# Kernel tuning notes

Measured on AMD Instinct MI355X. Metric: run time of the kernel, lower is better.

The kernel has to match this reference:

```python
import jax, jax.numpy as jnp
import numpy as np

EPS_ATTN = 1e-6
LN_EPS = 1e-5

def _layernorm(x, g, b):
    mu = jnp.mean(x, axis=-1, keepdims=True)
    var = jnp.var(x, axis=-1, keepdims=True)
    return (x - mu) * jax.lax.rsqrt(var + LN_EPS) * g + b

def _phi(x):
    return jax.nn.elu(x) + 1.0

def setup_inputs() -> dict:
    key = jax.random.key(0)
    ks = jax.random.split(key, 8)
    B, T, D, H = 2, 4096, 128, 128  # D = token_dim = d+1, H = hidden_dim
    s = 0.02
    return {
        "tokens": jax.random.normal(ks[0], (B, T, D), dtype=jnp.float32),
        "Wq": jax.random.normal(ks[1], (D, H), dtype=jnp.float32) * s,
        "Wk": jax.random.normal(ks[2], (D, H), dtype=jnp.float32) * s,
        "Wv": jax.random.normal(ks[3], (D, D), dtype=jnp.float32) * s,
        "Wg": jax.random.normal(ks[4], (D, D), dtype=jnp.float32) * s,
        "bg": jnp.zeros((D,), dtype=jnp.float32),
        "Wo": jax.random.normal(ks[5], (D, D), dtype=jnp.float32) * s,
        "g1": jnp.ones((D,), dtype=jnp.float32),
        "b1": jnp.zeros((D,), dtype=jnp.float32),
        "g2": jnp.ones((D,), dtype=jnp.float32),
        "b2": jnp.zeros((D,), dtype=jnp.float32),
    }

def reference(tokens, Wq, Wk, Wv, Wg, bg, Wo, g1, b1, g2, b2):
    x = _layernorm(tokens, g1, b1)                 # (b,t,m)
    Q = x @ Wq                                     # (b,t,h)
    K = x @ Wk                                     # (b,t,h)
    V = x @ Wv                                     # (b,t,m)
    G = jax.nn.sigmoid(x @ Wg + bg)                # (b,t,m)
    Vg = V * G
    Qp = _phi(Q)
    Kp = _phi(K)
    # causal linear attention via cumulative outer products
    kv = jnp.einsum('bth,btm->bthm', Kp, Vg)       # (b,t,h,m)
    S_kv = jnp.cumsum(kv, axis=1)
    S_k = jnp.cumsum(Kp, axis=1)
    numerator = jnp.einsum('bth,bthm->btm', Qp, S_kv)
    denom = jnp.maximum(jnp.einsum('bth,bth->bt', Qp, S_k), EPS_ATTN)
    attn_out = numerator / denom[..., None]
    out = tokens + (attn_out @ Wo) * 0.1
    return _layernorm(out, g2, b2)
```

## Files before the change

### kernel.cpp

```cpp
#include <hip/hip_runtime.h>
#include <math.h>

#define T_ 4096
#define D_ 128
#define NTOK 8192
#define CHUNK 64
#define NCB 64
#define NCH 128
#define LN_EPS 1e-5f
#define EPS_ATTN 1e-6f

typedef __attribute__((ext_vector_type(8))) short bf16x8;
typedef __attribute__((ext_vector_type(4))) short bf16x4;
typedef __attribute__((ext_vector_type(2))) short bf16x2;
typedef __attribute__((ext_vector_type(4))) float f32x4;

__device__ inline short f2bf(float f) {
  unsigned u = __builtin_bit_cast(unsigned, f);
  u += 0x7fffu + ((u >> 16) & 1u);
  return (short)(u >> 16);
}
__device__ inline float bf2f(short s) {
  unsigned u = ((unsigned)(unsigned short)s) << 16;
  return __builtin_bit_cast(float, u);
}
__device__ inline float phi_(float x) { return x > 0.f ? x + 1.f : __expf(x); }

__global__ __launch_bounds__(256) void k_prep(const float* __restrict__ in,
    const float* __restrict__ g, const float* __restrict__ b,
    short* __restrict__ xb) {
  const int w = threadIdx.x >> 6, l = threadIdx.x & 63;
  const int tok = blockIdx.x*4 + w;
  const float2 v = *(const float2*)&in[tok*D_ + l*2];
  float s = v.x + v.y, q = v.x*v.x + v.y*v.y;
  #pragma unroll
  for (int off = 32; off; off >>= 1) { s += __shfl_xor(s, off); q += __shfl_xor(q, off); }
  const float mean = s*(1.f/D_);
  const float r = rsqrtf(q*(1.f/D_) - mean*mean + LN_EPS);
  const float2 gg = *(const float2*)&g[l*2];
  const float2 bb = *(const float2*)&b[l*2];
  bf16x2 o;
  o.x = f2bf((v.x-mean)*r*gg.x + bb.x);
  o.y = f2bf((v.y-mean)*r*gg.y + bb.y);
  *(bf16x2*)&xb[tok*D_ + l*2] = o;
}

__global__ __launch_bounds__(256) void k_wprep(const float* __restrict__ Wq,
    const float* __restrict__ Wk, const float* __restrict__ Wv,
    const float* __restrict__ Wg, const float* __restrict__ Wo,
    short* __restrict__ WT) {
  const float* W = blockIdx.x==0?Wq: blockIdx.x==1?Wk: blockIdx.x==2?Wv: blockIdx.x==3?Wg:Wo;
  short* out = WT + blockIdx.x*D_*D_;
  __shared__ float lds[128][132];
  const int tid = threadIdx.x;
  #pragma unroll
  for (int it = 0; it < 16; ++it) {
    const int f = it*1024 + tid*4;
    const int k = f >> 7, n = f & 127;
    const float4 v = *(const float4*)&W[f];
    lds[k][n] = v.x; lds[k][n+1] = v.y; lds[k][n+2] = v.z; lds[k][n+3] = v.w;
  }
  __syncthreads();
  #pragma unroll
  for (int it = 0; it < 16; ++it) {
    const int f = it*1024 + tid*4;
    const int n = f >> 7, k = f & 127;
    bf16x4 o;
    o.x = f2bf(lds[k][n]);   o.y = f2bf(lds[k+1][n]);
    o.z = f2bf(lds[k+2][n]); o.w = f2bf(lds[k+3][n]);
    *(bf16x4*)&out[f] = o;
  }
}

__global__ __launch_bounds__(256) void k_qkvg(const short* __restrict__ xb,
    const short* __restrict__ WT,
    short* __restrict__ Qp, short* __restrict__ Kp, short* __restrict__ KpT,
    short* __restrict__ VT, short* __restrict__ GT) {
  const int m0 = blockIdx.x * 64;
  const int y = blockIdx.y;
  const int tid = threadIdx.x;
  __shared__ short xs[64][136];
  __shared__ short wsd[128][136];
  const short* W = WT + y*D_*D_;
  #pragma unroll
  for (int u = tid; u < 1024; u += 256) {
    const int r = u >> 4, c8 = (u & 15)*8;
    *(bf16x8*)&xs[r][c8] = *(const bf16x8*)&xb[(m0+r)*D_ + c8];
  }
  #pragma unroll
  for (int u = tid; u < 2048; u += 256) {
    const int r = u >> 4, c8 = (u & 15)*8;
    *(bf16x8*)&wsd[r][c8] = *(const bf16x8*)&W[r*D_ + c8];
  }
  __syncthreads();
  const int w = tid >> 6, l = tid & 63;
  const int i = l & 15, q = l >> 4;
  f32x4 acc[4][2];
  #pragma unroll
  for (int mt = 0; mt < 4; ++mt)
    #pragma unroll
    for (int nt = 0; nt < 2; ++nt) acc[mt][nt] = (f32x4){0.f,0.f,0.f,0.f};
  #pragma unroll
  for (int kk = 0; kk < 4; ++kk) {
    bf16x8 a[4], bfr[2];
    #pragma unroll
    for (int mt = 0; mt < 4; ++mt) a[mt] = *(const bf16x8*)&xs[mt*16+i][kk*32+q*8];
    #pragma unroll
    for (int nt = 0; nt < 2; ++nt) bfr[nt] = *(const bf16x8*)&wsd[w*32+nt*16+i][kk*32+q*8];
    #pragma unroll
    for (int mt = 0; mt < 4; ++mt)
      #pragma unroll
      for (int nt = 0; nt < 2; ++nt)
        acc[mt][nt] = __builtin_amdgcn_mfma_f32_16x16x32_bf16(a[mt], bfr[nt], acc[mt][nt], 0, 0, 0);
  }
  if (y == 0) {
    #pragma unroll
    for (int mt = 0; mt < 4; ++mt)
      #pragma unroll
      for (int nt = 0; nt < 2; ++nt) {
        const int h = w*32 + nt*16 + i;
        #pragma unroll
        for (int r = 0; r < 4; ++r) {
          const int t = m0 + mt*16 + 4*q + r;
          Qp[t*D_ + h] = f2bf(phi_(acc[mt][nt][r]));
        }
      }
  } else if (y == 1) {
    #pragma unroll
    for (int mt = 0; mt < 4; ++mt)
      #pragma unroll
      for (int nt = 0; nt < 2; ++nt) {
        const int h = w*32 + nt*16 + i;
        const int t0 = m0 + mt*16 + 4*q;
        bf16x4 o;
        #pragma unroll
        for (int r = 0; r < 4; ++r) {
          const float pv = phi_(acc[mt][nt][r]);
          const short bv = f2bf(pv);
          Kp[(t0+r)*D_ + h] = bv;
          o[r] = bv;
        }
        *(bf16x4*)&KpT[h*NTOK + t0] = o;
      }
  } else {
    short* dst = (y == 2) ? VT : GT;
    #pragma unroll
    for (int mt = 0; mt < 4; ++mt)
      #pragma unroll
      for (int nt = 0; nt < 2; ++nt) {
        const int h = w*32 + nt*16 + i;
        const int t0 = m0 + mt*16 + 4*q;
        bf16x4 o;
        #pragma unroll
        for (int r = 0; r < 4; ++r) o[r] = f2bf(acc[mt][nt][r]);
        *(bf16x4*)&dst[h*NTOK + t0] = o;
      }
  }
}

__global__ __launch_bounds__(256) void k_chunkkv(const short* __restrict__ KpT,
    const short* __restrict__ VT, const short* __restrict__ GT,
    const float* __restrict__ bg,
    float* __restrict__ KVT, float* __restrict__ Ksum) {
  const int c = blockIdx.x, hh = blockIdx.y;
  const int tid = threadIdx.x;
  const int tb = c*CHUNK;
  __shared__ short vgl[128][72];
  __shared__ short kpl[64][72];
  __shared__ float ksp[64][5];
  #pragma unroll
  for (int u = tid; u < 1024; u += 256) {
    const int d = u >> 3, c8 = (u & 7)*8;
    bf16x8 v  = *(const bf16x8*)&VT[d*NTOK + tb + c8];
    bf16x8 g8 = *(const bf16x8*)&GT[d*NTOK + tb + c8];
    const float bgd = bg[d];
    bf16x8 o;
    #pragma unroll
    for (int j = 0; j < 8; ++j) {
      const float gv = 1.f/(1.f + __expf(-(bf2f(g8[j]) + bgd)));
      o[j] = f2bf(bf2f(v[j]) * gv);
    }
    *(bf16x8*)&vgl[d][c8] = o;
  }
  #pragma unroll
  for (int u = tid; u < 512; u += 256) {
    const int h = u >> 3, c8 = (u & 7)*8;
    *(bf16x8*)&kpl[h][c8] = *(const bf16x8*)&KpT[(hh*64+h)*NTOK + tb + c8];
  }
  __syncthreads();
  const int w = tid >> 6, l = tid & 63, i = l & 15, q = l >> 4;
  f32x4 acc[2][4];
  #pragma unroll
  for (int mt = 0; mt < 2; ++mt)
    #pragma unroll
    for (int nt = 0; nt < 4; ++nt) acc[mt][nt] = (f32x4){0.f,0.f,0.f,0.f};
  #pragma unroll
  for (int kk = 0; kk < 2; ++kk) {
    bf16x8 a[2], bb[4];
    #pragma unroll
    for (int mt = 0; mt < 2; ++mt) a[mt] = *(const bf16x8*)&vgl[(2*w+mt)*16+i][kk*32+q*8];
    #pragma unroll
    for (int nt = 0; nt < 4; ++nt) bb[nt] = *(const bf16x8*)&kpl[nt*16+i][kk*32+q*8];
    #pragma unroll
    for (int mt = 0; mt < 2; ++mt)
      #pragma unroll
      for (int nt = 0; nt < 4; ++nt)
        acc[mt][nt] = __builtin_amdgcn_mfma_f32_16x16x32_bf16(a[mt], bb[nt], acc[mt][nt], 0, 0, 0);
  }
  float* KVc = KVT + (size_t)c*16384;
  #pragma unroll
  for (int mt = 0; mt < 2; ++mt)
    #pragma unroll
    for (int nt = 0; nt < 4; ++nt)
      #pragma unroll
      for (int r = 0; r < 4; ++r) {
        const int d = (2*w+mt)*16 + 4*q + r;
        const int h = hh*64 + nt*16 + i;
        KVc[d*128 + h] = acc[mt][nt][r];
      }
  {
    const int h = tid >> 2, part = tid & 3;
    float s = 0.f;
    #pragma unroll
    for (int t = 0; t < 16; ++t) s += bf2f(kpl[h][part*16 + t]);
    ksp[h][part] = s;
  }
  __syncthreads();
  if (tid < 64)
    Ksum[c*128 + hh*64 + tid] = ksp[tid][0]+ksp[tid][1]+ksp[tid][2]+ksp[tid][3];
}

__global__ __launch_bounds__(256) void k_prefix(const float* __restrict__ KVT,
    short* __restrict__ KVTb, float* __restrict__ Ksum) {
  const int tid = threadIdx.x;
  if (blockIdx.x < 128) {
    const int b = blockIdx.x >> 6;
    const int e = (blockIdx.x & 63)*256 + tid;
    const size_t base = (size_t)b*NCB*16384 + e;
    float run = 0.f;
    #pragma unroll 8
    for (int c = 0; c < NCB; ++c) {
      const float v = KVT[base + (size_t)c*16384];
      KVTb[base + (size_t)c*16384] = f2bf(run);
      run += v;
    }
  } else if (tid < 128) {
    const int b = blockIdx.x - 128;
    float run = 0.f;
    #pragma unroll 8
    for (int c = 0; c < NCB; ++c) {
      const int idx = (b*NCB + c)*128 + tid;
      const float v = Ksum[idx];
      Ksum[idx] = run;
      run += v;
    }
  }
}

__global__ __launch_bounds__(256) void k_scores(const short* __restrict__ Qp,
    const short* __restrict__ Kp, const float* __restrict__ Ksum,
    short* __restrict__ A, float* __restrict__ den) {
  const int c = blockIdx.x, tid = threadIdx.x;
  const int tb = c*CHUNK;
  __shared__ short qpl[64][136], kpl[64][136];
  __shared__ float ksl[128], rsl[64];
  #pragma unroll
  for (int u = tid; u < 1024; u += 256) {
    const int t = u >> 4, c8 = (u & 15)*8;
    *(bf16x8*)&qpl[t][c8] = *(const bf16x8*)&Qp[(tb+t)*D_ + c8];
    *(bf16x8*)&kpl[t][c8] = *(const bf16x8*)&Kp[(tb+t)*D_ + c8];
  }
  if (tid < 128) ksl[tid] = Ksum[c*128 + tid];
  __syncthreads();
  const int w = tid >> 6, l = tid & 63, i = l & 15, q = l >> 4;
  f32x4 acc[4];
  #pragma unroll
  for (int nt = 0; nt < 4; ++nt) acc[nt] = (f32x4){0.f,0.f,0.f,0.f};
  #pragma unroll
  for (int kk = 0; kk < 4; ++kk) {
    bf16x8 a = *(const bf16x8*)&qpl[w*16+i][kk*32+q*8];
    for (int nt = 0; nt <= w; ++nt) {
      bf16x8 bb = *(const bf16x8*)&kpl[nt*16+i][kk*32+q*8];
      acc[nt] = __builtin_amdgcn_mfma_f32_16x16x32_bf16(a, bb, acc[nt], 0, 0, 0);
    }
  }
  short* Ac = A + c*4096;
  float rs[4] = {0.f,0.f,0.f,0.f};
  #pragma unroll
  for (int nt = 0; nt < 4; ++nt) {
    #pragma unroll
    for (int r = 0; r < 4; ++r) {
      const int t = w*16 + 4*q + r;
      const int s = nt*16 + i;
      const float v = (nt <= w && s <= t) ? acc[nt][r] : 0.f;
      rs[r] += v;
      Ac[t*64 + s] = f2bf(v);
    }
  }
  #pragma unroll
  for (int r = 0; r < 4; ++r) {
    #pragma unroll
    for (int off = 1; off < 16; off <<= 1) rs[r] += __shfl_xor(rs[r], off);
  }
  if (i == 0) {
    #pragma unroll
    for (int r = 0; r < 4; ++r) rsl[w*16 + 4*q + r] = rs[r];
  }
  __syncthreads();
  if (tid < 64) {
    float dot = 0.f;
    #pragma unroll 8
    for (int h = 0; h < 128; ++h) dot += bf2f(qpl[tid][h]) * ksl[h];
    den[c*64 + tid] = rsl[tid] + dot;
  }
}

__global__ __launch_bounds__(256) void k_attnout(const short* __restrict__ Aintra,
    const short* __restrict__ Qp, const short* __restrict__ VT,
    const short* __restrict__ GT, const float* __restrict__ bg,
    const short* __restrict__ KVTb, const float* __restrict__ den,
    short* __restrict__ attn) {
  const int c = blockIdx.x, dh = blockIdx.y, tid = threadIdx.x;
  const int tb = c*CHUNK;
  __shared__ short at[64][200], bt[64][200];
  __shared__ float denl[64];
  const short* Ac = Aintra + c*4096;
  #pragma unroll
  for (int u = tid; u < 512; u += 256) {
    const int t = u >> 3, c8 = (u & 7)*8;
    *(bf16x8*)&at[t][c8] = *(const bf16x8*)&Ac[t*64 + c8];
  }
  #pragma unroll
  for (int u = tid; u < 1024; u += 256) {
    const int t = u >> 4, c8 = (u & 15)*8;
    *(bf16x8*)&at[t][64 + c8] = *(const bf16x8*)&Qp[(tb+t)*D_ + c8];
  }
  #pragma unroll
  for (int u = tid; u < 512; u += 256) {
    const int dd = u >> 3, c8 = (u & 7)*8;
    const int d = dh*64 + dd;
    bf16x8 v  = *(const bf16x8*)&VT[d*NTOK + tb + c8];
    bf16x8 g8 = *(const bf16x8*)&GT[d*NTOK + tb + c8];
    const float bgd = bg[d];
    bf16x8 o;
    #pragma unroll
    for (int j = 0; j < 8; ++j) {
      const float gv = 1.f/(1.f + __expf(-(bf2f(g8[j]) + bgd)));
      o[j] = f2bf(bf2f(v[j]) * gv);
    }
    *(bf16x8*)&bt[dd][c8] = o;
  }
  #pragma unroll
  for (int u = tid; u < 1024; u += 256) {
    const int dd = u >> 4, c8 = (u & 15)*8;
    *(bf16x8*)&bt[dd][64 + c8] = *(const bf16x8*)&KVTb[(size_t)c*16384 + (dh*64+dd)*128 + c8];
  }
  if (tid < 64) denl[tid] = den[c*64 + tid];
  __syncthreads();
  const int w = tid >> 6, l = tid & 63, i = l & 15, q = l >> 4;
  f32x4 acc[4];
  #pragma unroll
  for (int nt = 0; nt < 4; ++nt) acc[nt] = (f32x4){0.f,0.f,0.f,0.f};
  #pragma unroll
  for (int kk = 0; kk < 6; ++kk) {
    bf16x8 a = *(const bf16x8*)&at[w*16+i][kk*32+q*8];
    #pragma unroll
    for (int nt = 0; nt < 4; ++nt) {
      bf16x8 bb = *(const bf16x8*)&bt[nt*16+i][kk*32+q*8];
      acc[nt] = __builtin_amdgcn_mfma_f32_16x16x32_bf16(a, bb, acc[nt], 0, 0, 0);
    }
  }
  #pragma unroll
  for (int r = 0; r < 4; ++r) {
    const int t = w*16 + 4*q + r;
    const float inv = 1.f / fmaxf(denl[t], EPS_ATTN);
    #pragma unroll
    for (int nt = 0; nt < 4; ++nt)
      attn[(size_t)(tb+t)*D_ + dh*64 + nt*16 + i] = f2bf(acc[nt][r] * inv);
  }
}

__global__ __launch_bounds__(256) void k_outln2(const short* __restrict__ attn,
    const short* __restrict__ WoT, const float* __restrict__ tokens,
    const float* __restrict__ g2, const float* __restrict__ b2,
    float* __restrict__ out) {
  const int m0 = blockIdx.x*32, tid = threadIdx.x;
  __shared__ short al[32][136], wl[128][136];
  __shared__ float tl[32][132];
  __shared__ float suml[32][2], ssql[32][2];
  __shared__ float meanl[32], rstdl[32];
  __shared__ float gl[128], bl2[128];
  #pragma unroll
  for (int u = tid; u < 512; u += 256) {
    const int t = u >> 4, c8 = (u & 15)*8;
    *(bf16x8*)&al[t][c8] = *(const bf16x8*)&attn[(m0+t)*D_ + c8];
  }
  #pragma unroll
  for (int u = tid; u < 2048; u += 256) {
    const int n = u >> 4, c8 = (u & 15)*8;
    *(bf16x8*)&wl[n][c8] = *(const bf16x8*)&WoT[n*D_ + c8];
  }
  #pragma unroll
  for (int u = tid; u < 1024; u += 256) {
    const int t = u >> 5, c4 = (u & 31)*4;
    *(float4*)&tl[t][c4] = *(const float4*)&tokens[(m0+t)*D_ + c4];
  }
  if (tid < 128) { gl[tid] = g2[tid]; bl2[tid] = b2[tid]; }
  __syncthreads();
  const int w = tid >> 6, l = tid & 63, i = l & 15, q = l >> 4;
  const int mt = w >> 1, nh = w & 1;
  f32x4 acc[4];
  #pragma unroll
  for (int j = 0; j < 4; ++j) acc[j] = (f32x4){0.f,0.f,0.f,0.f};
  #pragma unroll
  for (int kk = 0; kk < 4; ++kk) {
    bf16x8 a = *(const bf16x8*)&al[mt*16+i][kk*32+q*8];
    #pragma unroll
    for (int j = 0; j < 4; ++j) {
      bf16x8 bb = *(const bf16x8*)&wl[(nh*4+j)*16+i][kk*32+q*8];
      acc[j] = __builtin_amdgcn_mfma_f32_16x16x32_bf16(a, bb, acc[j], 0, 0, 0);
    }
  }
  float p[4][4], ps[4], qs[4];
  #pragma unroll
  for (int r = 0; r < 4; ++r) {
    const int t = mt*16 + 4*q + r;
    ps[r] = 0.f; qs[r] = 0.f;
    #pragma unroll
    for (int j = 0; j < 4; ++j) {
      const int col = nh*64 + j*16 + i;
      const float v = tl[t][col] + 0.1f*acc[j][r];
      p[r][j] = v; ps[r] += v; qs[r] += v*v;
    }
  }
  #pragma unroll
  for (int r = 0; r < 4; ++r) {
    #pragma unroll
    for (int off = 1; off < 16; off <<= 1) {
      ps[r] += __shfl_xor(ps[r], off);
      qs[r] += __shfl_xor(qs[r], off);
    }
  }
  if (i == 0) {
    #pragma unroll
    for (int r = 0; r < 4; ++r) {
      suml[mt*16+4*q+r][nh] = ps[r];
      ssql[mt*16+4*q+r][nh] = qs[r];
    }
  }
  __syncthreads();
  if (tid < 32) {
    const float s = suml[tid][0] + suml[tid][1];
    const float qq = ssql[tid][0] + ssql[tid][1];
    const float mean = s*(1.f/D_);
    meanl[tid] = mean;
    rstdl[tid] = rsqrtf(qq*(1.f/D_) - mean*mean + LN_EPS);
  }
  __syncthreads();
  #pragma unroll
  for (int r = 0; r < 4; ++r) {
    const int t = mt*16 + 4*q + r;
    const float mean = meanl[t], rr = rstdl[t];
    #pragma unroll
    for (int j = 0; j < 4; ++j) {
      const int col = nh*64 + j*16 + i;
      out[(m0+t)*D_ + col] = (p[r][j]-mean)*rr*gl[col] + bl2[col];
    }
  }
}

extern "C" void kernel_launch(void* const* d_in, const int* in_sizes, int n_in,
                              void* d_out, int out_size, void* d_ws, size_t ws_size,
                              hipStream_t stream) {
  const float* tokens = (const float*)d_in[0];
  const float* Wq = (const float*)d_in[1];
  const float* Wk = (const float*)d_in[2];
  const float* Wv = (const float*)d_in[3];
  const float* Wg = (const float*)d_in[4];
  const float* bg = (const float*)d_in[5];
  const float* Wo = (const float*)d_in[6];
  const float* g1 = (const float*)d_in[7];
  const float* b1 = (const float*)d_in[8];
  const float* g2 = (const float*)d_in[9];
  const float* b2 = (const float*)d_in[10];

  char* base = (char*)d_ws;
  short* xb     = (short*)(base);
  short* Qp     = (short*)(base + (2u<<20));
  short* Kp     = (short*)(base + (4u<<20));
  short* KpT    = (short*)(base + (6u<<20));
  short* VT     = (short*)(base + (8u<<20));
  short* GT     = (short*)(base + (10u<<20));
  short* attn   = (short*)(base + (12u<<20));
  short* KVTb   = (short*)(base + (14u<<20));
  short* Aintra = (short*)(base + (18u<<20));
  short* WT     = (short*)(base + (19u<<20));
  float* den    = (float*)(base + (19u<<20) + (512u<<10));
  float* Ksum   = (float*)(base + (19u<<20) + (768u<<10));
  float* KVT    = (float*)(base + (20u<<20));

  short* WoT = WT + 4*D_*D_;

  k_prep<<<NTOK/4, 256, 0, stream>>>(tokens, g1, b1, xb);
  k_wprep<<<5, 256, 0, stream>>>(Wq, Wk, Wv, Wg, Wo, WT);
  k_qkvg<<<dim3(NTOK/64, 4), 256, 0, stream>>>(xb, WT, Qp, Kp, KpT, VT, GT);
  k_chunkkv<<<dim3(NCH, 2), 256, 0, stream>>>(KpT, VT, GT, bg, KVT, Ksum);
  k_prefix<<<130, 256, 0, stream>>>(KVT, KVTb, Ksum);
  k_scores<<<NCH, 256, 0, stream>>>(Qp, Kp, Ksum, Aintra, den);
  k_attnout<<<dim3(NCH, 2), 256, 0, stream>>>(Aintra, Qp, VT, GT, bg, KVTb, den, attn);
  k_outln2<<<NTOK/32, 256, 0, stream>>>(attn, WoT, tokens, g2, b2, (float*)d_out);
}
```

Measured before the change: 124.9 us.

## Fuse LayerNorm, weight prep, gating and scoring into fewer kernels

Result: faster. 120.3 us (-3.7%).

```diff
diff --git a/kernel.cpp b/kernel.cpp
--- a/kernel.cpp
+++ b/kernel.cpp
@@ -12,7 +12,6 @@
 
 typedef __attribute__((ext_vector_type(8))) short bf16x8;
 typedef __attribute__((ext_vector_type(4))) short bf16x4;
-typedef __attribute__((ext_vector_type(2))) short bf16x2;
 typedef __attribute__((ext_vector_type(4))) float f32x4;
 
 __device__ inline short f2bf(float f) {
@@ -26,93 +25,90 @@
 }
 __device__ inline float phi_(float x) { return x > 0.f ? x + 1.f : __expf(x); }
 
-__global__ __launch_bounds__(256) void k_prep(const float* __restrict__ in,
-    const float* __restrict__ g, const float* __restrict__ b,
-    short* __restrict__ xb) {
-  const int w = threadIdx.x >> 6, l = threadIdx.x & 63;
-  const int tok = blockIdx.x*4 + w;
-  const float2 v = *(const float2*)&in[tok*D_ + l*2];
-  float s = v.x + v.y, q = v.x*v.x + v.y*v.y;
-  #pragma unroll
-  for (int off = 32; off; off >>= 1) { s += __shfl_xor(s, off); q += __shfl_xor(q, off); }
-  const float mean = s*(1.f/D_);
-  const float r = rsqrtf(q*(1.f/D_) - mean*mean + LN_EPS);
-  const float2 gg = *(const float2*)&g[l*2];
-  const float2 bb = *(const float2*)&b[l*2];
-  bf16x2 o;
-  o.x = f2bf((v.x-mean)*r*gg.x + bb.x);
-  o.y = f2bf((v.y-mean)*r*gg.y + bb.y);
-  *(bf16x2*)&xb[tok*D_ + l*2] = o;
-}
-
-__global__ __launch_bounds__(256) void k_wprep(const float* __restrict__ Wq,
-    const float* __restrict__ Wk, const float* __restrict__ Wv,
-    const float* __restrict__ Wg, const float* __restrict__ Wo,
-    short* __restrict__ WT) {
-  const float* W = blockIdx.x==0?Wq: blockIdx.x==1?Wk: blockIdx.x==2?Wv: blockIdx.x==3?Wg:Wo;
-  short* out = WT + blockIdx.x*D_*D_;
-  __shared__ float lds[128][132];
-  const int tid = threadIdx.x;
-  #pragma unroll
-  for (int it = 0; it < 16; ++it) {
-    const int f = it*1024 + tid*4;
-    const int k = f >> 7, n = f & 127;
-    const float4 v = *(const float4*)&W[f];
-    lds[k][n] = v.x; lds[k][n+1] = v.y; lds[k][n+2] = v.z; lds[k][n+3] = v.w;
-  }
-  __syncthreads();
-  #pragma unroll
-  for (int it = 0; it < 16; ++it) {
-    const int f = it*1024 + tid*4;
-    const int n = f >> 7, k = f & 127;
-    bf16x4 o;
-    o.x = f2bf(lds[k][n]);   o.y = f2bf(lds[k+1][n]);
-    o.z = f2bf(lds[k+2][n]); o.w = f2bf(lds[k+3][n]);
-    *(bf16x4*)&out[f] = o;
-  }
-}
-
-__global__ __launch_bounds__(256) void k_qkvg(const short* __restrict__ xb,
-    const short* __restrict__ WT,
+__global__ __launch_bounds__(256) void k_qkvg(const float* __restrict__ tokens,
+    const float* __restrict__ Wq, const float* __restrict__ Wk,
+    const float* __restrict__ Wv, const float* __restrict__ Wg,
+    const float* __restrict__ g1, const float* __restrict__ b1,
+    const float* __restrict__ bg,
     short* __restrict__ Qp, short* __restrict__ Kp, short* __restrict__ KpT,
-    short* __restrict__ VT, short* __restrict__ GT) {
+    short* __restrict__ VgT) {
   const int m0 = blockIdx.x * 64;
   const int y = blockIdx.y;
   const int tid = threadIdx.x;
+  const int w = tid >> 6, l = tid & 63;
   __shared__ short xs[64][136];
   __shared__ short wsd[128][136];
-  const short* W = WT + y*D_*D_;
-  #pragma unroll
-  for (int u = tid; u < 1024; u += 256) {
-    const int r = u >> 4, c8 = (u & 15)*8;
-    *(bf16x8*)&xs[r][c8] = *(const bf16x8*)&xb[(m0+r)*D_ + c8];
-  }
-  #pragma unroll
-  for (int u = tid; u < 2048; u += 256) {
-    const int r = u >> 4, c8 = (u & 15)*8;
-    *(bf16x8*)&wsd[r][c8] = *(const bf16x8*)&W[r*D_ + c8];
-  }
-  __syncthreads();
-  const int w = tid >> 6, l = tid & 63;
+
+  {
+    const int half = l >> 5;
+    const int c4 = (l & 31) * 4;
+    float4 tv[8];
+    #pragma unroll
+    for (int it = 0; it < 8; ++it) {
+      const int t = m0 + w*16 + it*2 + half;
+      tv[it] = *(const float4*)&tokens[t*D_ + c4];
+    }
+    const float4 gg = *(const float4*)&g1[c4];
+    const float4 bb = *(const float4*)&b1[c4];
+    #pragma unroll
+    for (int it = 0; it < 8; ++it) {
+      const float4 v = tv[it];
+      float s = v.x+v.y+v.z+v.w;
+      float q = v.x*v.x+v.y*v.y+v.z*v.z+v.w*v.w;
+      #pragma unroll
+      for (int off = 1; off < 32; off <<= 1) {
+        s += __shfl_xor(s, off); q += __shfl_xor(q, off);
+      }
+      const float mean = s*(1.f/D_);
+      const float r = rsqrtf(q*(1.f/D_) - mean*mean + LN_EPS);
+      bf16x4 o;
+      o.x = f2bf((v.x-mean)*r*gg.x + bb.x);
+      o.y = f2bf((v.y-mean)*r*gg.y + bb.y);
+      o.z = f2bf((v.z-mean)*r*gg.z + bb.z);
+      o.w = f2bf((v.w-mean)*r*gg.w + bb.w);
+      *(bf16x4*)&xs[w*16 + it*2 + half][c4] = o;
+    }
+  }
+
+  auto stageW = [&](const float* __restrict__ W) {
+    #pragma unroll
+    for (int it = 0; it < 16; ++it) {
+      const int f = it*1024 + tid*4;
+      const int k = f >> 7, n = f & 127;
+      const float4 v = *(const float4*)&W[f];
+      wsd[n  ][k] = f2bf(v.x);
+      wsd[n+1][k] = f2bf(v.y);
+      wsd[n+2][k] = f2bf(v.z);
+      wsd[n+3][k] = f2bf(v.w);
+    }
+  };
+
   const int i = l & 15, q = l >> 4;
+  auto gemm = [&](f32x4 (*acc)[2]) {
+    #pragma unroll
+    for (int kk = 0; kk < 4; ++kk) {
+      bf16x8 a[4], bfr[2];
+      #pragma unroll
+      for (int mt = 0; mt < 4; ++mt) a[mt] = *(const bf16x8*)&xs[mt*16+i][kk*32+q*8];
+      #pragma unroll
+      for (int nt = 0; nt < 2; ++nt) bfr[nt] = *(const bf16x8*)&wsd[w*32+nt*16+i][kk*32+q*8];
+      #pragma unroll
+      for (int mt = 0; mt < 4; ++mt)
+        #pragma unroll
+        for (int nt = 0; nt < 2; ++nt)
+          acc[mt][nt] = __builtin_amdgcn_mfma_f32_16x16x32_bf16(a[mt], bfr[nt], acc[mt][nt], 0, 0, 0);
+    }
+  };
+
+  stageW(y == 0 ? Wq : (y == 1 ? Wk : Wv));
+  __syncthreads();
   f32x4 acc[4][2];
   #pragma unroll
   for (int mt = 0; mt < 4; ++mt)
     #pragma unroll
     for (int nt = 0; nt < 2; ++nt) acc[mt][nt] = (f32x4){0.f,0.f,0.f,0.f};
-  #pragma unroll
-  for (int kk = 0; kk < 4; ++kk) {
-    bf16x8 a[4], bfr[2];
-    #pragma unroll
-    for (int mt = 0; mt < 4; ++mt) a[mt] = *(const bf16x8*)&xs[mt*16+i][kk*32+q*8];
-    #pragma unroll
-    for (int nt = 0; nt < 2; ++nt) bfr[nt] = *(const bf16x8*)&wsd[w*32+nt*16+i][kk*32+q*8];
-    #pragma unroll
-    for (int mt = 0; mt < 4; ++mt)
-      #pragma unroll
-      for (int nt = 0; nt < 2; ++nt)
-        acc[mt][nt] = __builtin_amdgcn_mfma_f32_16x16x32_bf16(a[mt], bfr[nt], acc[mt][nt], 0, 0, 0);
-  }
+  gemm(acc);
+
   if (y == 0) {
     #pragma unroll
     for (int mt = 0; mt < 4; ++mt)
@@ -120,10 +116,8 @@
       for (int nt = 0; nt < 2; ++nt) {
         const int h = w*32 + nt*16 + i;
         #pragma unroll
-        for (int r = 0; r < 4; ++r) {
-          const int t = m0 + mt*16 + 4*q + r;
-          Qp[t*D_ + h] = f2bf(phi_(acc[mt][nt][r]));
-        }
+        for (int r = 0; r < 4; ++r)
+          Qp[(m0 + mt*16 + 4*q + r)*D_ + h] = f2bf(phi_(acc[mt][nt][r]));
       }
   } else if (y == 1) {
     #pragma unroll
@@ -135,32 +129,42 @@
         bf16x4 o;
         #pragma unroll
         for (int r = 0; r < 4; ++r) {
-          const float pv = phi_(acc[mt][nt][r]);
-          const short bv = f2bf(pv);
+          const short bv = f2bf(phi_(acc[mt][nt][r]));
           Kp[(t0+r)*D_ + h] = bv;
           o[r] = bv;
         }
         *(bf16x4*)&KpT[h*NTOK + t0] = o;
       }
   } else {
-    short* dst = (y == 2) ? VT : GT;
+    __syncthreads();
+    stageW(Wg);
+    __syncthreads();
+    f32x4 accg[4][2];
+    #pragma unroll
+    for (int mt = 0; mt < 4; ++mt)
+      #pragma unroll
+      for (int nt = 0; nt < 2; ++nt) accg[mt][nt] = (f32x4){0.f,0.f,0.f,0.f};
+    gemm(accg);
     #pragma unroll
     for (int mt = 0; mt < 4; ++mt)
       #pragma unroll
       for (int nt = 0; nt < 2; ++nt) {
         const int h = w*32 + nt*16 + i;
         const int t0 = m0 + mt*16 + 4*q;
+        const float bgd = bg[h];
         bf16x4 o;
         #pragma unroll
-        for (int r = 0; r < 4; ++r) o[r] = f2bf(acc[mt][nt][r]);
-        *(bf16x4*)&dst[h*NTOK + t0] = o;
+        for (int r = 0; r < 4; ++r) {
+          const float gv = 1.f/(1.f + __expf(-(accg[mt][nt][r] + bgd)));
+          o[r] = f2bf(acc[mt][nt][r] * gv);
+        }
+        *(bf16x4*)&VgT[h*NTOK + t0] = o;
       }
   }
 }
 
 __global__ __launch_bounds__(256) void k_chunkkv(const short* __restrict__ KpT,
-    const short* __restrict__ VT, const short* __restrict__ GT,
-    const float* __restrict__ bg,
+    const short* __restrict__ VgT,
     float* __restrict__ KVT, float* __restrict__ Ksum) {
   const int c = blockIdx.x, hh = blockIdx.y;
   const int tid = threadIdx.x;
@@ -171,16 +175,7 @@
   #pragma unroll
   for (int u = tid; u < 1024; u += 256) {
     const int d = u >> 3, c8 = (u & 7)*8;
-    bf16x8 v  = *(const bf16x8*)&VT[d*NTOK + tb + c8];
-    bf16x8 g8 = *(const bf16x8*)&GT[d*NTOK + tb + c8];
-    const float bgd = bg[d];
-    bf16x8 o;
-    #pragma unroll
-    for (int j = 0; j < 8; ++j) {
-      const float gv = 1.f/(1.f + __expf(-(bf2f(g8[j]) + bgd)));
-      o[j] = f2bf(bf2f(v[j]) * gv);
-    }
-    *(bf16x8*)&vgl[d][c8] = o;
+    *(bf16x8*)&vgl[d][c8] = *(const bf16x8*)&VgT[d*NTOK + tb + c8];
   }
   #pragma unroll
   for (int u = tid; u < 512; u += 256) {
@@ -230,8 +225,10 @@
     Ksum[c*128 + hh*64 + tid] = ksp[tid][0]+ksp[tid][1]+ksp[tid][2]+ksp[tid][3];
 }
 
-__global__ __launch_bounds__(256) void k_prefix(const float* __restrict__ KVT,
-    short* __restrict__ KVTb, float* __restrict__ Ksum) {
+__global__ __launch_bounds__(256) void k_prescore(const float* __restrict__ KVT,
+    short* __restrict__ KVTb, float* __restrict__ Ksum,
+    const short* __restrict__ Qp, const short* __restrict__ Kp,
+    short* __restrict__ A, float* __restrict__ rowsum) {
   const int tid = threadIdx.x;
   if (blockIdx.x < 128) {
     const int b = blockIdx.x >> 6;
@@ -244,33 +241,29 @@
       KVTb[base + (size_t)c*16384] = f2bf(run);
       run += v;
     }
-  } else if (tid < 128) {
-    const int b = blockIdx.x - 128;
+    return;
+  }
+  if (blockIdx.x == 128) {
+    const int b = tid >> 7, h = tid & 127;
     float run = 0.f;
     #pragma unroll 8
     for (int c = 0; c < NCB; ++c) {
-      const int idx = (b*NCB + c)*128 + tid;
+      const int idx = (b*NCB + c)*128 + h;
       const float v = Ksum[idx];
       Ksum[idx] = run;
       run += v;
     }
-  }
-}
-
-__global__ __launch_bounds__(256) void k_scores(const short* __restrict__ Qp,
-    const short* __restrict__ Kp, const float* __restrict__ Ksum,
-    short* __restrict__ A, float* __restrict__ den) {
-  const int c = blockIdx.x, tid = threadIdx.x;
+    return;
+  }
+  const int c = blockIdx.x - 129;
   const int tb = c*CHUNK;
   __shared__ short qpl[64][136], kpl[64][136];
-  __shared__ float ksl[128], rsl[64];
   #pragma unroll
   for (int u = tid; u < 1024; u += 256) {
     const int t = u >> 4, c8 = (u & 15)*8;
     *(bf16x8*)&qpl[t][c8] = *(const bf16x8*)&Qp[(tb+t)*D_ + c8];
     *(bf16x8*)&kpl[t][c8] = *(const bf16x8*)&Kp[(tb+t)*D_ + c8];
   }
-  if (tid < 128) ksl[tid] = Ksum[c*128 + tid];
   __syncthreads();
   const int w = tid >> 6, l = tid & 63, i = l & 15, q = l >> 4;
   f32x4 acc[4];
@@ -304,26 +297,18 @@
   }
   if (i == 0) {
     #pragma unroll
-    for (int r = 0; r < 4; ++r) rsl[w*16 + 4*q + r] = rs[r];
-  }
-  __syncthreads();
-  if (tid < 64) {
-    float dot = 0.f;
-    #pragma unroll 8
-    for (int h = 0; h < 128; ++h) dot += bf2f(qpl[tid][h]) * ksl[h];
-    den[c*64 + tid] = rsl[tid] + dot;
+    for (int r = 0; r < 4; ++r) rowsum[c*64 + w*16 + 4*q + r] = rs[r];
   }
 }
 
 __global__ __launch_bounds__(256) void k_attnout(const short* __restrict__ Aintra,
-    const short* __restrict__ Qp, const short* __restrict__ VT,
-    const short* __restrict__ GT, const float* __restrict__ bg,
-    const short* __restrict__ KVTb, const float* __restrict__ den,
-    short* __restrict__ attn) {
+    const short* __restrict__ Qp, const short* __restrict__ VgT,
+    const short* __restrict__ KVTb, const float* __restrict__ Ksum,
+    const float* __restrict__ rowsum, short* __restrict__ attn) {
   const int c = blockIdx.x, dh = blockIdx.y, tid = threadIdx.x;
   const int tb = c*CHUNK;
   __shared__ short at[64][200], bt[64][200];
-  __shared__ float denl[64];
+  __shared__ float ksl[128], dpart[64][4], denl[64];
   const short* Ac = Aintra + c*4096;
   #pragma unroll
   for (int u = tid; u < 512; u += 256) {
@@ -338,24 +323,25 @@
   #pragma unroll
   for (int u = tid; u < 512; u += 256) {
     const int dd = u >> 3, c8 = (u & 7)*8;
-    const int d = dh*64 + dd;
-    bf16x8 v  = *(const bf16x8*)&VT[d*NTOK + tb + c8];
-    bf16x8 g8 = *(const bf16x8*)&GT[d*NTOK + tb + c8];
-    const float bgd = bg[d];
-    bf16x8 o;
-    #pragma unroll
-    for (int j = 0; j < 8; ++j) {
-      const float gv = 1.f/(1.f + __expf(-(bf2f(g8[j]) + bgd)));
-      o[j] = f2bf(bf2f(v[j]) * gv);
-    }
-    *(bf16x8*)&bt[dd][c8] = o;
+    *(bf16x8*)&bt[dd][c8] = *(const bf16x8*)&VgT[(dh*64+dd)*NTOK + tb + c8];
   }
   #pragma unroll
   for (int u = tid; u < 1024; u += 256) {
     const int dd = u >> 4, c8 = (u & 15)*8;
     *(bf16x8*)&bt[dd][64 + c8] = *(const bf16x8*)&KVTb[(size_t)c*16384 + (dh*64+dd)*128 + c8];
   }
-  if (tid < 64) denl[tid] = den[c*64 + tid];
+  if (tid < 128) ksl[tid] = Ksum[c*128 + tid];
+  __syncthreads();
+  {
+    const int t = tid >> 2, part = tid & 3;
+    float dot = 0.f;
+    #pragma unroll
+    for (int h = 0; h < 32; ++h) dot += bf2f(at[t][64 + part*32 + h]) * ksl[part*32 + h];
+    dpart[t][part] = dot;
+  }
+  __syncthreads();
+  if (tid < 64)
+    denl[tid] = fmaxf(rowsum[c*64 + tid] + dpart[tid][0]+dpart[tid][1]+dpart[tid][2]+dpart[tid][3], EPS_ATTN);
   __syncthreads();
   const int w = tid >> 6, l = tid & 63, i = l & 15, q = l >> 4;
   f32x4 acc[4];
@@ -373,7 +359,7 @@
   #pragma unroll
   for (int r = 0; r < 4; ++r) {
     const int t = w*16 + 4*q + r;
-    const float inv = 1.f / fmaxf(denl[t], EPS_ATTN);
+    const float inv = 1.f / denl[t];
     #pragma unroll
     for (int nt = 0; nt < 4; ++nt)
       attn[(size_t)(tb+t)*D_ + dh*64 + nt*16 + i] = f2bf(acc[nt][r] * inv);
@@ -381,7 +367,7 @@
 }
 
 __global__ __launch_bounds__(256) void k_outln2(const short* __restrict__ attn,
-    const short* __restrict__ WoT, const float* __restrict__ tokens,
+    const float* __restrict__ Wo, const float* __restrict__ tokens,
     const float* __restrict__ g2, const float* __restrict__ b2,
     float* __restrict__ out) {
   const int m0 = blockIdx.x*32, tid = threadIdx.x;
@@ -396,9 +382,14 @@
     *(bf16x8*)&al[t][c8] = *(const bf16x8*)&attn[(m0+t)*D_ + c8];
   }
   #pragma unroll
-  for (int u = tid; u < 2048; u += 256) {
-    const int n = u >> 4, c8 = (u & 15)*8;
-    *(bf16x8*)&wl[n][c8] = *(const bf16x8*)&WoT[n*D_ + c8];
+  for (int it = 0; it < 16; ++it) {
+    const int f = it*1024 + tid*4;
+    const int k = f >> 7, n = f & 127;
+    const float4 v = *(const float4*)&Wo[f];
+    wl[n  ][k] = f2bf(v.x);
+    wl[n+1][k] = f2bf(v.y);
+    wl[n+2][k] = f2bf(v.z);
+    wl[n+3][k] = f2bf(v.w);
   }
   #pragma unroll
   for (int u = tid; u < 1024; u += 256) {
@@ -485,28 +476,21 @@
   const float* b2 = (const float*)d_in[10];
 
   char* base = (char*)d_ws;
-  short* xb     = (short*)(base);
-  short* Qp     = (short*)(base + (2u<<20));
-  short* Kp     = (short*)(base + (4u<<20));
-  short* KpT    = (short*)(base + (6u<<20));
-  short* VT     = (short*)(base + (8u<<20));
-  short* GT     = (short*)(base + (10u<<20));
-  short* attn   = (short*)(base + (12u<<20));
-  short* KVTb   = (short*)(base + (14u<<20));
-  short* Aintra = (short*)(base + (18u<<20));
-  short* WT     = (short*)(base + (19u<<20));
-  float* den    = (float*)(base + (19u<<20) + (512u<<10));
-  float* Ksum   = (float*)(base + (19u<<20) + (768u<<10));
-  float* KVT    = (float*)(base + (20u<<20));
-
-  short* WoT = WT + 4*D_*D_;
-
-  k_prep<<<NTOK/4, 256, 0, stream>>>(tokens, g1, b1, xb);
-  k_wprep<<<5, 256, 0, stream>>>(Wq, Wk, Wv, Wg, Wo, WT);
-  k_qkvg<<<dim3(NTOK/64, 4), 256, 0, stream>>>(xb, WT, Qp, Kp, KpT, VT, GT);
-  k_chunkkv<<<dim3(NCH, 2), 256, 0, stream>>>(KpT, VT, GT, bg, KVT, Ksum);
-  k_prefix<<<130, 256, 0, stream>>>(KVT, KVTb, Ksum);
-  k_scores<<<NCH, 256, 0, stream>>>(Qp, Kp, Ksum, Aintra, den);
-  k_attnout<<<dim3(NCH, 2), 256, 0, stream>>>(Aintra, Qp, VT, GT, bg, KVTb, den, attn);
-  k_outln2<<<NTOK/32, 256, 0, stream>>>(attn, WoT, tokens, g2, b2, (float*)d_out);
-}
+  short* Qp     = (short*)(base);
+  short* Kp     = (short*)(base + (2u<<20));
+  short* KpT    = (short*)(base + (4u<<20));
+  short* VgT    = (short*)(base + (6u<<20));
+  short* attn   = (short*)(base + (8u<<20));
+  short* KVTb   = (short*)(base + (10u<<20));
+  short* Aintra = (short*)(base + (14u<<20));
+  float* rowsum = (float*)(base + (15u<<20));
+  float* Ksum   = (float*)(base + (15u<<20) + (256u<<10));
+  float* KVT    = (float*)(base + (16u<<20));
+
+  k_qkvg<<<dim3(NTOK/64, 3), 256, 0, stream>>>(tokens, Wq, Wk, Wv, Wg, g1, b1, bg,
+                                               Qp, Kp, KpT, VgT);
+  k_chunkkv<<<dim3(NCH, 2), 256, 0, stream>>>(KpT, VgT, KVT, Ksum);
+  k_prescore<<<257, 256, 0, stream>>>(KVT, KVTb, Ksum, Qp, Kp, Aintra, rowsum);
+  k_attnout<<<dim3(NCH, 2), 256, 0, stream>>>(Aintra, Qp, VgT, KVTb, Ksum, rowsum, attn);
+  k_outln2<<<NTOK/32, 256, 0, stream>>>(attn, Wo, tokens, g2, b2, (float*)d_out);
+}
```
